# Performance work log

Hardware: AMD Instinct MI355X
Metric: run time of the kernel (lower is better)

## Reference

```python
import jax, jax.numpy as jnp
import numpy as np

L = 3        # message passing layers
ALPHA = 0.9  # self-information retention
TOPK = 4     # cross-edge neighbors
EPS = 1e-8


def setup_inputs() -> dict:
    key = jax.random.key(0)
    k1, k2, k3, k4 = jax.random.split(key, 4)
    B, C, N, K, A = 8, 128, 256, 96, 512
    features = jax.random.normal(k1, (B, C, N), jnp.float32)
    adj = (jax.random.uniform(k2, (B, N, K)) < 0.1).astype(jnp.float32)
    total_feats = jax.random.normal(k3, (A, C), jnp.float32)
    mem_adj = (jax.random.uniform(k4, (A, K)) < 0.1).astype(jnp.float32)
    return {"features": features, "adj": adj, "total_feats": total_feats, "mem_adj": mem_adj}


def _l2norm(x, axis):
    # F.normalize: x / max(||x||, 1e-12)
    return x / jnp.maximum(jnp.linalg.norm(x, axis=axis, keepdims=True), 1e-12)


def build_cross_incidence(X, mem_X):
    # X: (B,C,N) test features; mem_X: (B,A,C) memory features
    B, C, N = X.shape
    A = mem_X.shape[1]
    sim = jnp.einsum('bcn,bac->bna', _l2norm(X, 1), _l2norm(mem_X, 2))  # (B,N,A)
    knn = jax.lax.top_k(sim, TOPK)[1]                                   # (B,N,TOPK)
    E = N + A  # bidirectional
    H = jnp.zeros((B, N + A, E), X.dtype)
    n_ix = jnp.arange(N)
    # cross edge j contains test node j ...
    H = H.at[:, n_ix, n_ix].set(1.0)
    # ... and its topk memory neighbors (vectorized form of the per-batch scatter_)
    b_ix = jnp.arange(B)[:, None, None]
    H = H.at[b_ix, knn + N, n_ix[None, :, None]].set(1.0)
    # reverse edges: edge N+a contains memory node a and its topk test neighbors
    rev = jax.lax.top_k(jnp.swapaxes(sim, 1, 2), TOPK)[1]               # (B,A,TOPK)
    a_ix = jnp.arange(A)
    H = H.at[:, N + a_ix, N + a_ix].set(1.0)
    H = H.at[b_ix, rev, (N + a_ix)[None, :, None]].set(1.0)
    return H


def tf_mp(X, H):
    # X: (B,C,N), H: (B,N,M)
    B, C, N = X.shape
    d_e_inv = 1.0 / (H.sum(axis=1) + EPS)                 # (B,M), replaces diag_embed bmm
    W = jnp.einsum('bnm,bm,bkm->bnk', H, d_e_inv, H)      # clique expansion (B,N,N)
    I = jnp.eye(N, dtype=X.dtype)
    W_t = W + I
    d_is = 1.0 / jnp.sqrt(W_t.sum(axis=2) + EPS)          # (B,N)
    Amat = d_is[:, :, None] * W_t * d_is[:, None, :]      # D^-1/2 W~ D^-1/2
    A_pow = jnp.broadcast_to(I, (B, N, N))
    S = ALPHA * A_pow
    for l in range(1, L):
        A_pow = A_pow @ Amat
        S = S + ALPHA * (1.0 - ALPHA) ** l * A_pow
    A_pow = A_pow @ Amat
    S = S + (1.0 - ALPHA) ** L * A_pow
    return jnp.swapaxes(S @ jnp.swapaxes(X, 1, 2), 1, 2)  # (B,C,N)


def reference(features, adj, total_feats, mem_adj):
    B, C, N = features.shape
    A = total_feats.shape[0]
    K = adj.shape[2]
    mem_X = jnp.broadcast_to(total_feats[None], (B, A, C))
    mem_H = jnp.broadcast_to(mem_adj[None], (B, A, K))
    H_cross = build_cross_incidence(features, mem_X)      # (B, N+A, N+A)
    H_test = jnp.concatenate([adj, jnp.zeros((B, A, K), adj.dtype)], axis=1)
    H_mem = jnp.concatenate([jnp.zeros((B, N, K), adj.dtype), mem_H], axis=1)
    H_joint = jnp.concatenate([H_test, H_mem, H_cross], axis=2)  # (B, N+A, 2K+N+A)
    joint_X = jnp.concatenate([features, jnp.swapaxes(mem_X, 1, 2)], axis=2)  # (B,C,N+A)
    X_hat = tf_mp(joint_X, H_joint)[:, :, :N]
    # X_E = D_HE @ adj^T @ D_HV @ X_hat^T, via broadcasting instead of diag_embed
    inv_edge = 1.0 / jnp.clip(adj.sum(axis=1), EPS)                 # (B,K)
    inv_sqrt_node = 1.0 / jnp.sqrt(jnp.clip(adj.sum(axis=2), EPS))  # (B,N)
    X_E = inv_edge[:, :, None] * jnp.einsum('bnk,bn,bcn->bkc', adj, inv_sqrt_node, X_hat)
    return (X_hat, X_E)
```

## Files before the change

kernel.cpp:

```cpp
#include <hip/hip_runtime.h>

#define NB 8
#define NC 128
#define NN 256
#define NK 96
#define NA 512
#define NM 768

typedef __attribute__((ext_vector_type(8))) short bf16x8;
typedef __attribute__((ext_vector_type(4))) float f32x4;
typedef __attribute__((ext_vector_type(4))) unsigned short u16x4;

__device__ __forceinline__ float wave_reduce_add(float s) {
    for (int o = 32; o > 0; o >>= 1) s += __shfl_down(s, o, 64);
    return s;
}

__device__ __forceinline__ unsigned short f2bf(float x) {
    unsigned u = __float_as_uint(x);
    unsigned r = (u + 0x7FFFu + ((u >> 16) & 1u)) >> 16;
    return (unsigned short)r;
}
__device__ __forceinline__ float bf2f(unsigned short h) {
    return __uint_as_float((unsigned)h << 16);
}

#define NORM_BLKS (NA + NB * NN)
#define DEG_WAVES (NK + NB * NK + NB * NN)
__global__ __launch_bounds__(128) void k_normdeg(const float* __restrict__ tf,
                                                 const float* __restrict__ feat,
                                                 const float* __restrict__ mem_adj,
                                                 const float* __restrict__ adj,
                                                 float* __restrict__ memN_T,
                                                 float* __restrict__ tfT,
                                                 float* __restrict__ Xn,
                                                 float* __restrict__ dmem_inv,
                                                 float* __restrict__ sc_adj,
                                                 float* __restrict__ inv_edge,
                                                 float* __restrict__ isn) {
    __shared__ float p[2];
    int bi = blockIdx.x, c = threadIdx.x;
    if (bi < NA) {
        int a = bi;
        float v = tf[a * NC + c];
        float s = wave_reduce_add(v * v);
        if ((c & 63) == 0) p[c >> 6] = s;
        __syncthreads();
        float norm = sqrtf(p[0] + p[1]);
        memN_T[c * NA + a] = v / fmaxf(norm, 1e-12f);
        tfT[c * NA + a] = v;
    } else if (bi < NORM_BLKS) {
        int g = bi - NA;
        int b = g >> 8, n = g & 255;
        float v = feat[(b * NC + c) * NN + n];
        float s = wave_reduce_add(v * v);
        if ((c & 63) == 0) p[c >> 6] = s;
        __syncthreads();
        float norm = sqrtf(p[0] + p[1]);
        Xn[g * NC + c] = v / fmaxf(norm, 1e-12f);
    } else {
        int wid = (bi - NORM_BLKS) * 2 + (c >> 6);
        int lane = c & 63;
        if (wid < NK) {
            float s = 0.f;
            for (int a = lane; a < NA; a += 64) s += mem_adj[(size_t)a * NK + wid];
            s = wave_reduce_add(s);
            if (lane == 0) dmem_inv[wid] = 1.0f / (s + 1e-8f);
        } else if (wid < NK + NB * NK) {
            int w2 = wid - NK;
            int b = w2 / NK, k = w2 % NK;
            float s = 0.f;
            for (int n = lane; n < NN; n += 64) s += adj[(size_t)(b * NN + n) * NK + k];
            s = wave_reduce_add(s);
            if (lane == 0) {
                sc_adj[w2] = 1.0f / (s + 1e-8f);
                inv_edge[w2] = 1.0f / fmaxf(s, 1e-8f);
            }
        } else if (wid < DEG_WAVES) {
            int w3 = wid - NK - NB * NK;
            const float* row = adj + (size_t)w3 * NK;
            float s = (lane < NK) ? row[lane] : 0.f;
            if (lane + 64 < NK) s += row[lane + 64];
            s = wave_reduce_add(s);
            if (lane == 0) isn[w3] = 1.0f / sqrtf(fmaxf(s, 1e-8f));
        }
    }
}

__global__ __launch_bounds__(512) void k_sim(const float* __restrict__ Xn,
                                             const float* __restrict__ memN_T,
                                             float* __restrict__ sim,
                                             float* __restrict__ simT) {
    __shared__ float xr[8][NC];
    int g0 = blockIdx.x * 8;
    int b = g0 >> 8, n0 = g0 & 255;
    int t = threadIdx.x;
    for (int i = t; i < 8 * NC; i += 512) xr[i / NC][i % NC] = Xn[g0 * NC + i];
    __syncthreads();
    float acc[8] = {0, 0, 0, 0, 0, 0, 0, 0};
    int a = t;
    for (int c = 0; c < NC; c++) {
        float m = memN_T[c * NA + a];
#pragma unroll
        for (int r = 0; r < 8; r++) acc[r] += xr[r][c] * m;
    }
#pragma unroll
    for (int r = 0; r < 8; r++) sim[(size_t)(g0 + r) * NA + a] = acc[r];
    float* tp = simT + ((size_t)(b * NA + a)) * NN + n0;
    f32x4 v0, v1;
    v0[0] = acc[0]; v0[1] = acc[1]; v0[2] = acc[2]; v0[3] = acc[3];
    v1[0] = acc[4]; v1[1] = acc[5]; v1[2] = acc[6]; v1[3] = acc[7];
    *(f32x4*)tp = v0;
    *(f32x4*)(tp + 4) = v1;
}

__device__ __forceinline__ unsigned long long pack_key(float v, unsigned idx) {
    unsigned u = __float_as_uint(v);
    u = (u & 0x80000000u) ? ~u : (u | 0x80000000u);
    return ((unsigned long long)u << 32) | (unsigned long long)(0xFFFFFFFFu - idx);
}

__device__ __forceinline__ void ins4(unsigned long long v, unsigned long long* k) {
    if (v > k[3]) {
        if (v > k[1]) {
            if (v > k[0]) { k[3] = k[2]; k[2] = k[1]; k[1] = k[0]; k[0] = v; }
            else         { k[3] = k[2]; k[2] = k[1]; k[1] = v; }
        } else {
            if (v > k[2]) { k[3] = k[2]; k[2] = v; }
            else          { k[3] = v; }
        }
    }
}

__device__ __forceinline__ void merge_top4(unsigned long long* k) {
#pragma unroll
    for (int d = 1; d < 64; d <<= 1) {
        unsigned long long p0 = __shfl_xor(k[0], d, 64);
        unsigned long long p1 = __shfl_xor(k[1], d, 64);
        unsigned long long p2 = __shfl_xor(k[2], d, 64);
        unsigned long long p3 = __shfl_xor(k[3], d, 64);
        unsigned long long c0 = k[0] > p3 ? k[0] : p3;
        unsigned long long c1 = k[1] > p2 ? k[1] : p2;
        unsigned long long c2 = k[2] > p1 ? k[2] : p1;
        unsigned long long c3 = k[3] > p0 ? k[3] : p0;
        unsigned long long d0 = c0 > c2 ? c0 : c2, d2 = c0 > c2 ? c2 : c0;
        unsigned long long d1 = c1 > c3 ? c1 : c3, d3 = c1 > c3 ? c3 : c1;
        k[0] = d0 > d1 ? d0 : d1; k[1] = d0 > d1 ? d1 : d0;
        k[2] = d2 > d3 ? d2 : d3; k[3] = d2 > d3 ? d3 : d2;
    }
}

__global__ __launch_bounds__(256) void k_knnrev(const float* __restrict__ sim,
                                                const float* __restrict__ simT,
                                                float* __restrict__ W) {
    int wid = (blockIdx.x * 256 + threadIdx.x) >> 6;
    int lane = threadIdx.x & 63;
    unsigned long long k[4] = {0, 0, 0, 0};
    const float cval = 1.0f / (5.0f + 1e-8f);
    int b, rr0;
    if (wid < NB * NN) {
        b = wid >> 8;
        rr0 = wid & 255;
        const float* row = sim + (size_t)wid * NA;
#pragma unroll
        for (int t = 0; t < NA / 64; t++) {
            int a = lane + 64 * t;
            ins4(pack_key(row[a], (unsigned)a), k);
        }
        merge_top4(k);
        int rr[5];
        rr[0] = rr0;
#pragma unroll
        for (int t = 0; t < 4; t++) rr[t + 1] = NN + (int)(0xFFFFFFFFu - (unsigned)k[t]);
        if (lane < 25) {
            int i = lane / 5, j = lane - i * 5;
            atomicAdd(W + (size_t)b * NM * NM + (size_t)rr[i] * NM + rr[j], cval);
        }
    } else {
        int w2 = wid - NB * NN;
        b = w2 >> 9;
        rr0 = NN + (w2 & 511);
        const float* row = simT + (size_t)w2 * NN;
#pragma unroll
        for (int t = 0; t < NN / 64; t++) {
            int n = lane + 64 * t;
            ins4(pack_key(row[n], (unsigned)n), k);
        }
        merge_top4(k);
        int rr[5];
        rr[0] = rr0;
#pragma unroll
        for (int t = 0; t < 4; t++) rr[t + 1] = (int)(0xFFFFFFFFu - (unsigned)k[t]);
        if (lane < 25) {
            int i = lane / 5, j = lane - i * 5;
            atomicAdd(W + (size_t)b * NM * NM + (size_t)rr[i] * NM + rr[j], cval);
        }
    }
}

__global__ __launch_bounds__(256) void k_wblocks(const float* __restrict__ mem_adj,
                                                 const float* __restrict__ dmem_inv,
                                                 const float* __restrict__ adj,
                                                 const float* __restrict__ sc_adj,
                                                 float* __restrict__ W) {
    __shared__ float ta[16][NK + 1];
    __shared__ float tb[16][NK + 1];
    int bi = blockIdx.x, tid = threadIdx.x;
    int tx = tid & 15, ty = tid >> 4;
    if (bi < 1024) {
        int a0 = (bi >> 5) * 16, a1 = (bi & 31) * 16;
        for (int i = tid; i < 16 * NK; i += 256) {
            int r = i / NK, j = i % NK;
            ta[r][j] = mem_adj[(a0 + r) * NK + j] * dmem_inv[j];
            tb[r][j] = mem_adj[(a1 + r) * NK + j];
        }
        __syncthreads();
        float s = 0.f;
        for (int j = 0; j < NK; j++) s += ta[ty][j] * tb[tx][j];
        int row = NN + a0 + ty, col = NN + a1 + tx;
        for (int b = 0; b < NB; b++) W[(size_t)b * NM * NM + (size_t)row * NM + col] = s;
    } else if (bi < 3072) {
        int t = bi - 1024;
        int n1 = (t & 15) * 16, n0 = ((t >> 4) & 15) * 16, b = t >> 8;
        const float* adjb = adj + (size_t)b * NN * NK;
        const float* scb = sc_adj + b * NK;
        for (int i = tid; i < 16 * NK; i += 256) {
            int r = i / NK, j = i % NK;
            ta[r][j] = adjb[(n0 + r) * NK + j] * scb[j];
            tb[r][j] = adjb[(n1 + r) * NK + j];
        }
        __syncthreads();
        float s = 0.f;
        for (int j = 0; j < NK; j++) s += ta[ty][j] * tb[tx][j];
        W[(size_t)b * NM * NM + (size_t)(n0 + ty) * NM + (n1 + tx)] = s;
    } else {
        int t = bi - 3072;
        int b = t >> 6;
        f32x4 z; z[0] = 0.f; z[1] = 0.f; z[2] = 0.f; z[3] = 0.f;
#pragma unroll
        for (int q = 0; q < 4; q++) {
            int v = (t & 63) * 1024 + q * 256 + tid;
            int row, col4;
            if (v < 32768) { row = v >> 7; col4 = 64 + (v & 127); }
            else { int v2 = v - 32768; row = 256 + (v2 >> 6); col4 = v2 & 63; }
            *(f32x4*)(W + (size_t)b * NM * NM + (size_t)row * NM + col4 * 4) = z;
        }
    }
}

__global__ __launch_bounds__(256) void k_w16dis(const float* __restrict__ W,
                                                unsigned short* __restrict__ W16,
                                                float* __restrict__ dis) {
    int wid = (blockIdx.x * 256 + threadIdx.x) >> 6;
    int lane = threadIdx.x & 63;
    if (wid >= NB * NM) return;
    const float* row = W + (size_t)wid * NM;
    unsigned short* row16 = W16 + (size_t)wid * NM;
    float s = 0.f;
#pragma unroll
    for (int t = 0; t < 3; t++) {
        int e = (lane + t * 64) * 4;
        f32x4 v = *(const f32x4*)(row + e);
        s += (v[0] + v[1]) + (v[2] + v[3]);
        u16x4 o;
        o[0] = f2bf(v[0]); o[1] = f2bf(v[1]); o[2] = f2bf(v[2]); o[3] = f2bf(v[3]);
        *(u16x4*)(row16 + e) = o;
    }
    s = wave_reduce_add(s);
    if (lane == 0) dis[wid] = 1.0f / sqrtf(s + 1.0f + 1e-8f);
}

__global__ void k_y0(const float* __restrict__ feat, const float* __restrict__ tfT,
                     const float* __restrict__ dis, unsigned short* __restrict__ Z0,
                     float* __restrict__ Xh) {
    int bc = blockIdx.x;
    int b = bc >> 7, c = bc & 127;
    for (int m = threadIdx.x; m < NM; m += 256) {
        float v = (m < NN) ? feat[(size_t)bc * NN + m] : tfT[(size_t)c * NA + (m - NN)];
        Z0[(size_t)bc * NM + m] = f2bf(dis[b * NM + m] * v);
        Xh[(size_t)bc * NM + m] = 0.9f * v;
    }
}

__global__ __launch_bounds__(256) void k_prop(const unsigned short* __restrict__ W16,
                                              const float* __restrict__ dis,
                                              const unsigned short* __restrict__ Zin,
                                              unsigned short* __restrict__ Zout,
                                              float* __restrict__ Xh, float coef) {
    int b = blockIdx.z;
    int m0 = blockIdx.x * 32;
    int c0 = blockIdx.y * 64;
    int tid = threadIdx.x;
    int w = tid >> 6, l = tid & 63;
    int wm = w >> 1, wc = w & 1;
    int lr = l & 15, lg = l >> 4;

    const unsigned short* Ap = W16 + ((size_t)b * NM + m0 + wm * 16 + lr) * NM + lg * 8;
    const unsigned short* Bp = Zin + ((size_t)b * NC + c0 + wc * 32 + lr) * NM + lg * 8;

    f32x4 acc[2];
#pragma unroll
    for (int f = 0; f < 2; f++) { acc[f][0] = 0.f; acc[f][1] = 0.f; acc[f][2] = 0.f; acc[f][3] = 0.f; }

    bf16x8 a0 = *(const bf16x8*)(Ap);
    bf16x8 b0[2];
#pragma unroll
    for (int f = 0; f < 2; f++) b0[f] = *(const bf16x8*)(Bp + (size_t)(f * 16) * NM);

    for (int k0 = 0; k0 < NM - 32; k0 += 32) {
        bf16x8 a1 = *(const bf16x8*)(Ap + k0 + 32);
        bf16x8 b1[2];
#pragma unroll
        for (int f = 0; f < 2; f++) b1[f] = *(const bf16x8*)(Bp + (size_t)(f * 16) * NM + k0 + 32);
#pragma unroll
        for (int f = 0; f < 2; f++)
            acc[f] = __builtin_amdgcn_mfma_f32_16x16x32_bf16(a0, b0[f], acc[f], 0, 0, 0);
        a0 = a1;
#pragma unroll
        for (int f = 0; f < 2; f++) b0[f] = b1[f];
    }
#pragma unroll
    for (int f = 0; f < 2; f++)
        acc[f] = __builtin_amdgcn_mfma_f32_16x16x32_bf16(a0, b0[f], acc[f], 0, 0, 0);

    int mb = m0 + wm * 16 + lg * 4;
    f32x4 dv = *(const f32x4*)(dis + b * NM + mb);
#pragma unroll
    for (int f = 0; f < 2; f++) {
        int c = c0 + wc * 32 + f * 16 + lr;
        size_t off = ((size_t)b * NC + c) * NM + mb;
        u16x4 zi = *(const u16x4*)(Zin + off);
        f32x4 xh = *(const f32x4*)(Xh + off);
        u16x4 zo;
#pragma unroll
        for (int r = 0; r < 4; r++) {
            float o = dv[r] * (acc[f][r] + bf2f(zi[r]));
            xh[r] += coef * o;
            zo[r] = f2bf(dv[r] * o);
        }
        *(f32x4*)(Xh + off) = xh;
        *(u16x4*)(Zout + off) = zo;
    }
}

__global__ __launch_bounds__(256) void k_prop_last(const unsigned short* __restrict__ W16,
                                                   const float* __restrict__ dis,
                                                   const unsigned short* __restrict__ Zin,
                                                   const float* __restrict__ Xh,
                                                   float* __restrict__ out_xhat, float coef) {
    int b = blockIdx.z;
    int m0 = blockIdx.x * 32;
    int c0 = blockIdx.y * 64;
    int tid = threadIdx.x;
    int w = tid >> 6, l = tid & 63;
    int wm = w >> 1, wc = w & 1;
    int lr = l & 15, lg = l >> 4;

    const unsigned short* Ap = W16 + ((size_t)b * NM + m0 + wm * 16 + lr) * NM + lg * 8;
    const unsigned short* Bp = Zin + ((size_t)b * NC + c0 + wc * 32 + lr) * NM + lg * 8;

    f32x4 acc[2];
#pragma unroll
    for (int f = 0; f < 2; f++) { acc[f][0] = 0.f; acc[f][1] = 0.f; acc[f][2] = 0.f; acc[f][3] = 0.f; }

    bf16x8 a0 = *(const bf16x8*)(Ap);
    bf16x8 b0[2];
#pragma unroll
    for (int f = 0; f < 2; f++) b0[f] = *(const bf16x8*)(Bp + (size_t)(f * 16) * NM);

    for (int k0 = 0; k0 < NM - 32; k0 += 32) {
        bf16x8 a1 = *(const bf16x8*)(Ap + k0 + 32);
        bf16x8 b1[2];
#pragma unroll
        for (int f = 0; f < 2; f++) b1[f] = *(const bf16x8*)(Bp + (size_t)(f * 16) * NM + k0 + 32);
#pragma unroll
        for (int f = 0; f < 2; f++)
            acc[f] = __builtin_amdgcn_mfma_f32_16x16x32_bf16(a0, b0[f], acc[f], 0, 0, 0);
        a0 = a1;
#pragma unroll
        for (int f = 0; f < 2; f++) b0[f] = b1[f];
    }
#pragma unroll
    for (int f = 0; f < 2; f++)
        acc[f] = __builtin_amdgcn_mfma_f32_16x16x32_bf16(a0, b0[f], acc[f], 0, 0, 0);

    int mb = m0 + wm * 16 + lg * 4;
    f32x4 dv = *(const f32x4*)(dis + b * NM + mb);
#pragma unroll
    for (int f = 0; f < 2; f++) {
        int c = c0 + wc * 32 + f * 16 + lr;
        size_t offM = ((size_t)b * NC + c) * NM + mb;
        u16x4 zi = *(const u16x4*)(Zin + offM);
        f32x4 xh = *(const f32x4*)(Xh + offM);
        f32x4 ov;
#pragma unroll
        for (int r = 0; r < 4; r++) {
            float o = dv[r] * (acc[f][r] + bf2f(zi[r]));
            ov[r] = xh[r] + coef * o;
        }
        *(f32x4*)(out_xhat + ((size_t)b * NC + c) * NN + mb) = ov;
    }
}

__global__ __launch_bounds__(256) void k_xe(const float* __restrict__ Xhat,
                                            const float* __restrict__ adj,
                                            const float* __restrict__ isn,
                                            const float* __restrict__ inv_edge,
                                            float* __restrict__ outE) {
    __shared__ float ta[16][17];
    __shared__ float tz[16][17];
    int b = blockIdx.z;
    int k0 = blockIdx.y * 16;
    int c0 = blockIdx.x * 16;
    int tx = threadIdx.x & 15;
    int ty = threadIdx.x >> 4;
    float acc = 0.f;
    for (int n0 = 0; n0 < NN; n0 += 16) {
        int n = n0 + ty;
        ta[ty][tx] = adj[(size_t)(b * NN + n) * NK + k0 + tx] * isn[b * NN + n];
        tz[ty][tx] = Xhat[((size_t)b * NC + c0 + ty) * NN + n0 + tx];
        __syncthreads();
#pragma unroll
        for (int nn = 0; nn < 16; nn++) acc += ta[nn][ty] * tz[tx][nn];
        __syncthreads();
    }
    int k = k0 + ty, c = c0 + tx;
    outE[(size_t)(b * NK + k) * NC + c] = inv_edge[b * NK + k] * acc;
}

extern "C" void kernel_launch(void* const* d_in, const int* in_sizes, int n_in,
                              void* d_out, int out_size, void* d_ws, size_t ws_size,
                              hipStream_t stream) {
    (void)in_sizes; (void)n_in; (void)out_size; (void)ws_size;
    const float* features = (const float*)d_in[0];
    const float* adj      = (const float*)d_in[1];
    const float* tf       = (const float*)d_in[2];
    const float* mem_adj  = (const float*)d_in[3];
    float* out_xhat = (float*)d_out;
    float* out_xe   = out_xhat + (size_t)NB * NC * NN;

    float* p = (float*)d_ws;
    float* memN_T  = p; p += (size_t)NC * NA;
    float* tfT     = p; p += (size_t)NC * NA;
    float* Xn      = p; p += (size_t)NB * NN * NC;
    float* sim     = p; p += (size_t)NB * NN * NA;
    float* simT    = p; p += (size_t)NB * NN * NA;
    float* sc_adj  = p; p += NB * NK;
    float* inv_edge= p; p += NB * NK;
    float* dmem_inv= p; p += NK;
    float* isn     = p; p += NB * NN;
    float* dis     = p; p += NB * NM;
    float* W       = p; p += (size_t)NB * NM * NM;
    float* Xh      = p; p += (size_t)NB * NC * NM;
    unsigned short* W16 = (unsigned short*)p;
    unsigned short* Z0  = W16 + (size_t)NB * NM * NM;
    unsigned short* Z1  = Z0 + (size_t)NB * NC * NM;

    k_normdeg<<<NORM_BLKS + (DEG_WAVES + 1) / 2, 128, 0, stream>>>(
        tf, features, mem_adj, adj, memN_T, tfT, Xn, dmem_inv, sc_adj, inv_edge, isn);
    k_sim<<<NB * NN / 8, 512, 0, stream>>>(Xn, memN_T, sim, simT);
    k_wblocks<<<3584, 256, 0, stream>>>(mem_adj, dmem_inv, adj, sc_adj, W);
    k_knnrev<<<(NB * NN + NB * NA) / 4, 256, 0, stream>>>(sim, simT, W);
    k_w16dis<<<NB * NM / 4, 256, 0, stream>>>(W, W16, dis);
    k_y0<<<NB * NC, 256, 0, stream>>>(features, tfT, dis, Z0, Xh);
    dim3 pg(NM / 32, NC / 64, NB);
    k_prop<<<pg, 256, 0, stream>>>(W16, dis, Z0, Z1, Xh, 0.09f);
    k_prop<<<pg, 256, 0, stream>>>(W16, dis, Z1, Z0, Xh, 0.009f);
    dim3 pl(NN / 32, NC / 64, NB);
    k_prop_last<<<pl, 256, 0, stream>>>(W16, dis, Z0, Xh, out_xhat, 0.001f);
    k_xe<<<dim3(NC / 16, NK / 16, NB), 256, 0, stream>>>(out_xhat, adj, isn, inv_edge, out_xe);
}
```

Before: 118.8 us.

## Fuse similarity and W-block kernels; shrink Xhat accumulator to test nodes only

Merges the similarity GEMM kernel and the W block-construction kernel into one launch with block-index dispatch, so the independent work shares one grid. The similarity part now runs 256-thread blocks, each computing two memory columns per thread. Separately, the Xh accumulator is sized to only the first NN nodes, because only those columns reach the output. This removes reads and writes of the unused memory-node columns in the propagation kernels. One fewer launch and less traffic, at the cost of some branchiness in the fused kernel.

```diff
diff --git a/kernel.cpp b/kernel.cpp
--- a/kernel.cpp
+++ b/kernel.cpp
@@ -87,31 +87,91 @@
     }
 }
 
-__global__ __launch_bounds__(512) void k_sim(const float* __restrict__ Xn,
-                                             const float* __restrict__ memN_T,
-                                             float* __restrict__ sim,
-                                             float* __restrict__ simT) {
-    __shared__ float xr[8][NC];
-    int g0 = blockIdx.x * 8;
-    int b = g0 >> 8, n0 = g0 & 255;
-    int t = threadIdx.x;
-    for (int i = t; i < 8 * NC; i += 512) xr[i / NC][i % NC] = Xn[g0 * NC + i];
-    __syncthreads();
-    float acc[8] = {0, 0, 0, 0, 0, 0, 0, 0};
-    int a = t;
-    for (int c = 0; c < NC; c++) {
-        float m = memN_T[c * NA + a];
-#pragma unroll
-        for (int r = 0; r < 8; r++) acc[r] += xr[r][c] * m;
-    }
-#pragma unroll
-    for (int r = 0; r < 8; r++) sim[(size_t)(g0 + r) * NA + a] = acc[r];
-    float* tp = simT + ((size_t)(b * NA + a)) * NN + n0;
-    f32x4 v0, v1;
-    v0[0] = acc[0]; v0[1] = acc[1]; v0[2] = acc[2]; v0[3] = acc[3];
-    v1[0] = acc[4]; v1[1] = acc[5]; v1[2] = acc[6]; v1[3] = acc[7];
-    *(f32x4*)tp = v0;
-    *(f32x4*)(tp + 4) = v1;
+__global__ __launch_bounds__(256) void k_simwb(const float* __restrict__ Xn,
+                                               const float* __restrict__ memN_T,
+                                               const float* __restrict__ mem_adj,
+                                               const float* __restrict__ dmem_inv,
+                                               const float* __restrict__ adj,
+                                               const float* __restrict__ sc_adj,
+                                               float* __restrict__ sim,
+                                               float* __restrict__ simT,
+                                               float* __restrict__ W) {
+    __shared__ float smem[2 * 16 * (NK + 1)];
+    int bi = blockIdx.x, tid = threadIdx.x;
+    int tx = tid & 15, ty = tid >> 4;
+    if (bi < 256) {
+        float (*xr)[NC] = (float(*)[NC])smem;
+        int g0 = bi * 8;
+        int b = g0 >> 8, n0 = g0 & 255;
+        for (int i = tid; i < 8 * NC; i += 256) xr[i >> 7][i & 127] = Xn[(size_t)g0 * NC + i];
+        __syncthreads();
+        float acc0[8] = {0, 0, 0, 0, 0, 0, 0, 0};
+        float acc1[8] = {0, 0, 0, 0, 0, 0, 0, 0};
+        int a0 = tid, a1 = tid + 256;
+        for (int c = 0; c < NC; c++) {
+            float m0 = memN_T[c * NA + a0];
+            float m1 = memN_T[c * NA + a1];
+#pragma unroll
+            for (int r = 0; r < 8; r++) { acc0[r] += xr[r][c] * m0; acc1[r] += xr[r][c] * m1; }
+        }
+#pragma unroll
+        for (int r = 0; r < 8; r++) {
+            sim[(size_t)(g0 + r) * NA + a0] = acc0[r];
+            sim[(size_t)(g0 + r) * NA + a1] = acc1[r];
+        }
+        float* tp0 = simT + ((size_t)(b * NA + a0)) * NN + n0;
+        float* tp1 = simT + ((size_t)(b * NA + a1)) * NN + n0;
+        f32x4 u, v;
+        u[0] = acc0[0]; u[1] = acc0[1]; u[2] = acc0[2]; u[3] = acc0[3];
+        v[0] = acc0[4]; v[1] = acc0[5]; v[2] = acc0[6]; v[3] = acc0[7];
+        *(f32x4*)tp0 = u; *(f32x4*)(tp0 + 4) = v;
+        u[0] = acc1[0]; u[1] = acc1[1]; u[2] = acc1[2]; u[3] = acc1[3];
+        v[0] = acc1[4]; v[1] = acc1[5]; v[2] = acc1[6]; v[3] = acc1[7];
+        *(f32x4*)tp1 = u; *(f32x4*)(tp1 + 4) = v;
+    } else if (bi < 1280) {
+        float (*ta)[NK + 1] = (float(*)[NK + 1])smem;
+        float (*tb)[NK + 1] = (float(*)[NK + 1])(smem + 16 * (NK + 1));
+        int t = bi - 256;
+        int a0 = (t >> 5) * 16, a1 = (t & 31) * 16;
+        for (int i = tid; i < 16 * NK; i += 256) {
+            int r = i / NK, j = i % NK;
+            ta[r][j] = mem_adj[(a0 + r) * NK + j] * dmem_inv[j];
+            tb[r][j] = mem_adj[(a1 + r) * NK + j];
+        }
+        __syncthreads();
+        float s = 0.f;
+        for (int j = 0; j < NK; j++) s += ta[ty][j] * tb[tx][j];
+        int row = NN + a0 + ty, col = NN + a1 + tx;
+        for (int b = 0; b < NB; b++) W[(size_t)b * NM * NM + (size_t)row * NM + col] = s;
+    } else if (bi < 3328) {
+        float (*ta)[NK + 1] = (float(*)[NK + 1])smem;
+        float (*tb)[NK + 1] = (float(*)[NK + 1])(smem + 16 * (NK + 1));
+        int t = bi - 1280;
+        int n1 = (t & 15) * 16, n0 = ((t >> 4) & 15) * 16, b = t >> 8;
+        const float* adjb = adj + (size_t)b * NN * NK;
+        const float* scb = sc_adj + b * NK;
+        for (int i = tid; i < 16 * NK; i += 256) {
+            int r = i / NK, j = i % NK;
+            ta[r][j] = adjb[(n0 + r) * NK + j] * scb[j];
+            tb[r][j] = adjb[(n1 + r) * NK + j];
+        }
+        __syncthreads();
+        float s = 0.f;
+        for (int j = 0; j < NK; j++) s += ta[ty][j] * tb[tx][j];
+        W[(size_t)b * NM * NM + (size_t)(n0 + ty) * NM + (n1 + tx)] = s;
+    } else {
+        int t = bi - 3328;
+        int b = t >> 6;
+        f32x4 z; z[0] = 0.f; z[1] = 0.f; z[2] = 0.f; z[3] = 0.f;
+#pragma unroll
+        for (int q = 0; q < 4; q++) {
+            int v = (t & 63) * 1024 + q * 256 + tid;
+            int row, col4;
+            if (v < 32768) { row = v >> 7; col4 = 64 + (v & 127); }
+            else { int v2 = v - 32768; row = 256 + (v2 >> 6); col4 = v2 & 63; }
+            *(f32x4*)(W + (size_t)b * NM * NM + (size_t)row * NM + col4 * 4) = z;
+        }
+    }
 }
 
 __device__ __forceinline__ unsigned long long pack_key(float v, unsigned idx) {
@@ -157,10 +217,10 @@
     int lane = threadIdx.x & 63;
     unsigned long long k[4] = {0, 0, 0, 0};
     const float cval = 1.0f / (5.0f + 1e-8f);
-    int b, rr0;
+    int b, rr[5];
     if (wid < NB * NN) {
         b = wid >> 8;
-        rr0 = wid & 255;
+        rr[0] = wid & 255;
         const float* row = sim + (size_t)wid * NA;
 #pragma unroll
         for (int t = 0; t < NA / 64; t++) {
@@ -168,18 +228,12 @@
             ins4(pack_key(row[a], (unsigned)a), k);
         }
         merge_top4(k);
-        int rr[5];
-        rr[0] = rr0;
 #pragma unroll
         for (int t = 0; t < 4; t++) rr[t + 1] = NN + (int)(0xFFFFFFFFu - (unsigned)k[t]);
-        if (lane < 25) {
-            int i = lane / 5, j = lane - i * 5;
-            atomicAdd(W + (size_t)b * NM * NM + (size_t)rr[i] * NM + rr[j], cval);
-        }
     } else {
         int w2 = wid - NB * NN;
         b = w2 >> 9;
-        rr0 = NN + (w2 & 511);
+        rr[0] = NN + (w2 & 511);
         const float* row = simT + (size_t)w2 * NN;
 #pragma unroll
         for (int t = 0; t < NN / 64; t++) {
@@ -187,64 +241,12 @@
             ins4(pack_key(row[n], (unsigned)n), k);
         }
         merge_top4(k);
-        int rr[5];
-        rr[0] = rr0;
 #pragma unroll
         for (int t = 0; t < 4; t++) rr[t + 1] = (int)(0xFFFFFFFFu - (unsigned)k[t]);
-        if (lane < 25) {
-            int i = lane / 5, j = lane - i * 5;
-            atomicAdd(W + (size_t)b * NM * NM + (size_t)rr[i] * NM + rr[j], cval);
-        }
-    }
-}
-
-__global__ __launch_bounds__(256) void k_wblocks(const float* __restrict__ mem_adj,
-                                                 const float* __restrict__ dmem_inv,
-                                                 const float* __restrict__ adj,
-                                                 const float* __restrict__ sc_adj,
-                                                 float* __restrict__ W) {
-    __shared__ float ta[16][NK + 1];
-    __shared__ float tb[16][NK + 1];
-    int bi = blockIdx.x, tid = threadIdx.x;
-    int tx = tid & 15, ty = tid >> 4;
-    if (bi < 1024) {
-        int a0 = (bi >> 5) * 16, a1 = (bi & 31) * 16;
-        for (int i = tid; i < 16 * NK; i += 256) {
-            int r = i / NK, j = i % NK;
-            ta[r][j] = mem_adj[(a0 + r) * NK + j] * dmem_inv[j];
-            tb[r][j] = mem_adj[(a1 + r) * NK + j];
-        }
-        __syncthreads();
-        float s = 0.f;
-        for (int j = 0; j < NK; j++) s += ta[ty][j] * tb[tx][j];
-        int row = NN + a0 + ty, col = NN + a1 + tx;
-        for (int b = 0; b < NB; b++) W[(size_t)b * NM * NM + (size_t)row * NM + col] = s;
-    } else if (bi < 3072) {
-        int t = bi - 1024;
-        int n1 = (t & 15) * 16, n0 = ((t >> 4) & 15) * 16, b = t >> 8;
-        const float* adjb = adj + (size_t)b * NN * NK;
-        const float* scb = sc_adj + b * NK;
-        for (int i = tid; i < 16 * NK; i += 256) {
-            int r = i / NK, j = i % NK;
-            ta[r][j] = adjb[(n0 + r) * NK + j] * scb[j];
-            tb[r][j] = adjb[(n1 + r) * NK + j];
-        }
-        __syncthreads();
-        float s = 0.f;
-        for (int j = 0; j < NK; j++) s += ta[ty][j] * tb[tx][j];
-        W[(size_t)b * NM * NM + (size_t)(n0 + ty) * NM + (n1 + tx)] = s;
-    } else {
-        int t = bi - 3072;
-        int b = t >> 6;
-        f32x4 z; z[0] = 0.f; z[1] = 0.f; z[2] = 0.f; z[3] = 0.f;
-#pragma unroll
-        for (int q = 0; q < 4; q++) {
-            int v = (t & 63) * 1024 + q * 256 + tid;
-            int row, col4;
-            if (v < 32768) { row = v >> 7; col4 = 64 + (v & 127); }
-            else { int v2 = v - 32768; row = 256 + (v2 >> 6); col4 = v2 & 63; }
-            *(f32x4*)(W + (size_t)b * NM * NM + (size_t)row * NM + col4 * 4) = z;
-        }
+    }
+    if (lane < 25) {
+        int i = lane / 5, j = lane - i * 5;
+        atomicAdd(W + (size_t)b * NM * NM + (size_t)rr[i] * NM + rr[j], cval);
     }
 }
 
@@ -278,7 +280,7 @@
     for (int m = threadIdx.x; m < NM; m += 256) {
         float v = (m < NN) ? feat[(size_t)bc * NN + m] : tfT[(size_t)c * NA + (m - NN)];
         Z0[(size_t)bc * NM + m] = f2bf(dis[b * NM + m] * v);
-        Xh[(size_t)bc * NM + m] = 0.9f * v;
+        if (m < NN) Xh[(size_t)bc * NN + m] = 0.9f * v;
     }
 }
 
@@ -325,20 +327,23 @@
 
     int mb = m0 + wm * 16 + lg * 4;
     f32x4 dv = *(const f32x4*)(dis + b * NM + mb);
+    bool doXh = (m0 < NN);
 #pragma unroll
     for (int f = 0; f < 2; f++) {
         int c = c0 + wc * 32 + f * 16 + lr;
         size_t off = ((size_t)b * NC + c) * NM + mb;
         u16x4 zi = *(const u16x4*)(Zin + off);
-        f32x4 xh = *(const f32x4*)(Xh + off);
         u16x4 zo;
+        f32x4 xh;
+        size_t offh = ((size_t)b * NC + c) * NN + mb;
+        if (doXh) xh = *(const f32x4*)(Xh + offh);
 #pragma unroll
         for (int r = 0; r < 4; r++) {
             float o = dv[r] * (acc[f][r] + bf2f(zi[r]));
-            xh[r] += coef * o;
+            if (doXh) xh[r] += coef * o;
             zo[r] = f2bf(dv[r] * o);
         }
-        *(f32x4*)(Xh + off) = xh;
+        if (doXh) *(f32x4*)(Xh + offh) = xh;
         *(u16x4*)(Zout + off) = zo;
     }
 }
@@ -391,7 +396,7 @@
         int c = c0 + wc * 32 + f * 16 + lr;
         size_t offM = ((size_t)b * NC + c) * NM + mb;
         u16x4 zi = *(const u16x4*)(Zin + offM);
-        f32x4 xh = *(const f32x4*)(Xh + offM);
+        f32x4 xh = *(const f32x4*)(Xh + ((size_t)b * NC + c) * NN + mb);
         f32x4 ov;
 #pragma unroll
         for (int r = 0; r < 4; r++) {
@@ -451,15 +456,15 @@
     float* isn     = p; p += NB * NN;
     float* dis     = p; p += NB * NM;
     float* W       = p; p += (size_t)NB * NM * NM;
-    float* Xh      = p; p += (size_t)NB * NC * NM;
+    float* Xh      = p; p += (size_t)NB * NC * NN;
     unsigned short* W16 = (unsigned short*)p;
     unsigned short* Z0  = W16 + (size_t)NB * NM * NM;
     unsigned short* Z1  = Z0 + (size_t)NB * NC * NM;
 
     k_normdeg<<<NORM_BLKS + (DEG_WAVES + 1) / 2, 128, 0, stream>>>(
         tf, features, mem_adj, adj, memN_T, tfT, Xn, dmem_inv, sc_adj, inv_edge, isn);
-    k_sim<<<NB * NN / 8, 512, 0, stream>>>(Xn, memN_T, sim, simT);
-    k_wblocks<<<3584, 256, 0, stream>>>(mem_adj, dmem_inv, adj, sc_adj, W);
+    k_simwb<<<3840, 256, 0, stream>>>(Xn, memN_T, mem_adj, dmem_inv, adj, sc_adj,
+                                      sim, simT, W);
     k_knnrev<<<(NB * NN + NB * NA) / 4, 256, 0, stream>>>(sim, simT, W);
     k_w16dis<<<NB * NM / 4, 256, 0, stream>>>(W, W16, dis);
     k_y0<<<NB * NC, 256, 0, stream>>>(features, tfT, dis, Z0, Xh);
```

Result: faster. 109.6 us (-7.7%).
